# Optimization experiments

Measured on AMD Instinct MI355X. Metric: run time of the kernel, lower is better.

The kernel has to match this reference:

```python
import jax, jax.numpy as jnp
import numpy as np

N_NODES = 100000
N_EDGES = 1600000
IN_DIM = 23
HID_DIM = 128
OUT_DIM = 64
NUM_GRAPHS = 64
EPS = 1e-12


def setup_inputs() -> dict:
    key = jax.random.key(0)
    ks = jax.random.split(key, 8)
    feat_0 = jax.random.normal(ks[0], (N_NODES, IN_DIM), dtype=jnp.float32)
    W1 = jax.random.normal(ks[1], (IN_DIM, HID_DIM), dtype=jnp.float32) * 0.1
    b1 = jax.random.normal(ks[2], (HID_DIM,), dtype=jnp.float32) * 0.1
    W2 = jax.random.normal(ks[3], (HID_DIM, OUT_DIM), dtype=jnp.float32) * 0.1
    b2 = jax.random.normal(ks[4], (OUT_DIM,), dtype=jnp.float32) * 0.1
    src = jax.random.randint(ks[5], (N_EDGES,), 0, N_NODES, dtype=jnp.int64 if jax.config.jax_enable_x64 else jnp.int32)
    dst = jax.random.randint(ks[6], (N_EDGES,), 0, N_NODES, dtype=src.dtype)
    graph_ids = jnp.sort(jax.random.randint(ks[7], (N_NODES,), 0, NUM_GRAPHS, dtype=src.dtype))
    return {"feat_0": feat_0, "W1": W1, "b1": b1, "W2": W2, "b2": b2,
            "src": src, "dst": dst, "graph_ids": graph_ids}


def _sage_gcn(h, src, dst, W, b):
    # DGL SAGEConv with aggregator_type='gcn':
    # h_neigh[v] = (sum_{u->v} h[u] + h[v]) / (in_deg(v) + 1); out = h_neigh @ W + b
    n = h.shape[0]
    agg = jax.ops.segment_sum(h[src], dst, num_segments=n)          # [N, d]
    deg = jax.ops.segment_sum(jnp.ones_like(dst, dtype=h.dtype), dst, num_segments=n)
    h_neigh = (agg + h) / (deg + 1.0)[:, None]
    return h_neigh @ W + b


def reference(feat_0, W1, b1, W2, b2, src, dst, graph_ids):
    # layer 1 + relu + L2 row-normalize (dropout omitted: eval mode)
    h = _sage_gcn(feat_0, src, dst, W1, b1)
    h = jax.nn.relu(h)
    norm = jnp.maximum(jnp.linalg.norm(h, axis=1, keepdims=True), EPS)
    h = h / norm
    # output layer
    h = _sage_gcn(h, src, dst, W2, b2)
    # dgl.mean_nodes: per-graph mean over nodes
    gsum = jax.ops.segment_sum(h, graph_ids, num_segments=NUM_GRAPHS)  # [G, out]
    cnt = jax.ops.segment_sum(jnp.ones((h.shape[0],), h.dtype), graph_ids, num_segments=NUM_GRAPHS)
    return gsum / jnp.maximum(cnt, 1.0)[:, None]
```

## Files before the change

### kernel.cpp

```cpp
#include <hip/hip_runtime.h>

#define IN_DIM 23
#define HID 128
#define OUTD 64
#define NGR 64
#define NXCD 8
#define FB_DIM 32
#define PH_STRIDE 136
#define A2_BLOCKS 2048
#define NB 256
#define CAP 8192
#define CHUNK 4096

typedef __attribute__((ext_vector_type(8))) short bf16x8;
typedef __attribute__((ext_vector_type(4))) float f32x4;
typedef __attribute__((ext_vector_type(2))) float f32x2;

static __device__ __forceinline__ unsigned xcd_id() {
    unsigned x;
    asm volatile("s_getreg_b32 %0, hwreg(20, 0, 32)" : "=s"(x));
    return x & (NXCD - 1);
}

static __device__ __forceinline__ unsigned short f2bf(float x) {
    unsigned u = __float_as_uint(x);
    unsigned r = (u + 0x7FFFu + ((u >> 16) & 1u)) >> 16;
    return (unsigned short)r;
}
static __device__ __forceinline__ float bf2f(unsigned short u) {
    return __uint_as_float((unsigned)u << 16);
}

static __device__ __forceinline__ unsigned enc_fp8(float x) {
    float a = fabsf(x);
    unsigned s = (__float_as_uint(x) >> 31) << 7;
    if (!(a > 0.f)) return s;
    a = fminf(a, 448.f);
    int eb; float fr = frexpf(a, &eb);
    int E = eb - 1;
    int code;
    if (E < -6) code = (int)rintf(ldexpf(a, 9));
    else        code = ((E + 7) << 3) + (int)rintf(ldexpf(fr, 4)) - 8;
    code = min(code, 0x7E);
    return s | (unsigned)code;
}

#if __has_builtin(__builtin_amdgcn_cvt_pk_fp8_f32)
static __device__ __forceinline__ unsigned enc4_fp8(float a, float b,
                                                    float c, float d) {
    int r = __builtin_amdgcn_cvt_pk_fp8_f32(a, b, 0, false);
    r = __builtin_amdgcn_cvt_pk_fp8_f32(c, d, r, true);
    return (unsigned)r;
}
#else
static __device__ __forceinline__ unsigned enc4_fp8(float a, float b,
                                                    float c, float d) {
    return enc_fp8(a) | (enc_fp8(b) << 8) | (enc_fp8(c) << 16)
         | (enc_fp8(d) << 24);
}
#endif

#if __has_builtin(__builtin_amdgcn_cvt_pk_f32_fp8)
static __device__ __forceinline__ void dec_pk(unsigned u, f32x2& lo, f32x2& hi) {
    lo = __builtin_amdgcn_cvt_pk_f32_fp8((int)u, false);
    hi = __builtin_amdgcn_cvt_pk_f32_fp8((int)u, true);
}
#else
static __device__ __forceinline__ float dec1_fp8(unsigned b) {
    unsigned s = (b & 0x80u) << 24;
    unsigned em = b & 0x7Fu;
    float f = __uint_as_float(s | ((em << 20) + 0x3C000000u));
    if ((b & 0x78u) == 0)
        f = 2.f * f - __uint_as_float(s | 0x3C800000u);
    return f;
}
static __device__ __forceinline__ void dec_pk(unsigned u, f32x2& lo, f32x2& hi) {
    lo[0] = dec1_fp8(u & 0xFF);        lo[1] = dec1_fp8((u >> 8) & 0xFF);
    hi[0] = dec1_fp8((u >> 16) & 0xFF); hi[1] = dec1_fp8(u >> 24);
}
#endif

__global__ __launch_bounds__(256) void k_featb(
    const float* __restrict__ feat0, unsigned short* __restrict__ featb,
    int n_nodes)
{
    int i = blockIdx.x * 256 + threadIdx.x;
    if (i >= n_nodes * FB_DIM) return;
    int v = i >> 5, d = i & (FB_DIM - 1);
    float x = (d < IN_DIM) ? feat0[(size_t)v * IN_DIM + d] : 0.f;
    featb[i] = f2bf(x);
}

__global__ __launch_bounds__(256) void k_wprep(
    const float* __restrict__ W1, const float* __restrict__ W2,
    unsigned short* __restrict__ W1t, unsigned short* __restrict__ W2t)
{
    int i = blockIdx.x * 256 + threadIdx.x;
    if (i < HID * 32) {
        int h = i >> 5, d = i & 31;
        W1t[i] = f2bf((d < IN_DIM) ? W1[d * HID + h] : 0.f);
    } else if (i < HID * 32 + OUTD * HID) {
        int j = i - HID * 32;
        int o = j >> 7, k = j & 127;
        W2t[j] = f2bf(W2[k * OUTD + o]);
    }
}

__global__ __launch_bounds__(256) void k_bin(
    const int* __restrict__ src, const int* __restrict__ dst,
    unsigned* __restrict__ brec, int* __restrict__ bcur,
    int n_edges, int n_nodes)
{
    __shared__ int cnt[NB], offs[NB], cur[NB];
    __shared__ unsigned stage[CHUNK];
    int t = threadIdx.x;
    int e0 = blockIdx.x * CHUNK;
    int e1 = min(e0 + CHUNK, n_edges);
    int myb[16];
    unsigned myrec[16];
    cnt[t] = 0;
    __syncthreads();
#pragma unroll
    for (int k = 0; k < 16; ++k) {
        int e = e0 + k * 256 + t;
        myb[k] = -1;
        if (e < e1) {
            int u = src[e], v = dst[e];
            int b = (v * NB) / n_nodes;
            int vlo = (b * n_nodes + NB - 1) / NB;
            myb[k] = b;
            myrec[k] = (unsigned)u | ((unsigned)(v - vlo) << 17);
            atomicAdd(&cnt[b], 1);
        }
    }
    __syncthreads();
    int c = cnt[t];
    offs[t] = c;
    __syncthreads();
    for (int off = 1; off < NB; off <<= 1) {
        int v = (t >= off) ? offs[t - off] : 0;
        __syncthreads();
        offs[t] += v;
        __syncthreads();
    }
    int excl = offs[t] - c;
    __syncthreads();
    offs[t] = excl;
    cur[t] = excl;
    __syncthreads();
#pragma unroll
    for (int k = 0; k < 16; ++k) {
        if (myb[k] >= 0) {
            int slot = atomicAdd(&cur[myb[k]], 1);
            stage[slot] = myrec[k];
        }
    }
    __syncthreads();
    int cc = cnt[t];
    int gb = 0;
    if (cc > 0) gb = atomicAdd(&bcur[t], cc);
    if (gb + cc > CAP) cc = max(0, CAP - gb);
    unsigned* dp = brec + (size_t)t * CAP + gb;
    int sb = offs[t];
    for (int k = 0; k < cc; ++k) dp[k] = stage[sb + k];
}

__global__ __launch_bounds__(NB) void k_bscan(
    const int* __restrict__ bcur, int* __restrict__ bbase,
    int* __restrict__ rowstart, const int* __restrict__ gids,
    float* __restrict__ gcnt, int n_nodes, int n_edges)
{
    __shared__ int s[NB];
    int t = threadIdx.x;
    int c = min(bcur[t], CAP);
    s[t] = c;
    __syncthreads();
    for (int off = 1; off < NB; off <<= 1) {
        int v = (t >= off) ? s[t - off] : 0;
        __syncthreads();
        s[t] += v;
        __syncthreads();
    }
    bbase[t] = s[t] - c;
    if (t == 0) rowstart[n_nodes] = n_edges;
    if (t < NGR) {
        int g = t;
        int lo = 0, hi = n_nodes;
        while (lo < hi) { int m = (lo + hi) >> 1; if (gids[m] < g) lo = m + 1; else hi = m; }
        int lb = lo;
        lo = 0; hi = n_nodes;
        while (lo < hi) { int m = (lo + hi) >> 1; if (gids[m] < g + 1) lo = m + 1; else hi = m; }
        gcnt[g] = (float)(lo - lb);
    }
}

__global__ __launch_bounds__(256) void k_csr(
    const unsigned* __restrict__ brec, const int* __restrict__ bcur,
    const int* __restrict__ bbase, int* __restrict__ rowstart,
    int* __restrict__ eidx, int n_nodes)
{
    __shared__ int hist[512], scr[256];
    int b = blockIdx.x, t = threadIdx.x;
    int vlo = (b * n_nodes + NB - 1) / NB;
    int vhi = ((b + 1) * n_nodes + NB - 1) / NB;
    int nn = vhi - vlo;
    int bcnt = min(bcur[b], CAP);
    int base = bbase[b];
    for (int i = t; i < nn; i += 256) hist[i] = 0;
    __syncthreads();
    const unsigned* rec = brec + (size_t)b * CAP;
    for (int r = t; r < bcnt; r += 256)
        atomicAdd(&hist[rec[r] >> 17], 1);
    __syncthreads();
    int i0 = 2 * t, i1 = i0 + 1;
    int a0 = (i0 < nn) ? hist[i0] : 0;
    int a1 = (i1 < nn) ? hist[i1] : 0;
    int s2 = a0 + a1;
    scr[t] = s2;
    __syncthreads();
    for (int off = 1; off < 256; off <<= 1) {
        int v = (t >= off) ? scr[t - off] : 0;
        __syncthreads();
        scr[t] += v;
        __syncthreads();
    }
    int excl = scr[t] - s2;
    __syncthreads();
    if (i0 < nn) hist[i0] = excl;
    if (i1 < nn) hist[i1] = excl + a0;
    __syncthreads();
    for (int i = t; i < nn; i += 256) rowstart[vlo + i] = base + hist[i];
    __syncthreads();
    for (int r = t; r < bcnt; r += 256) {
        unsigned e = rec[r];
        int pos = atomicAdd(&hist[e >> 17], 1);
        eidx[base + pos] = (int)(e & 0x1FFFFu);
    }
}

__global__ __launch_bounds__(256) void k_agg1(
    const int* __restrict__ rowstart, const int* __restrict__ eidx,
    const unsigned* __restrict__ fbd, unsigned* __restrict__ hnbd, int n_nodes)
{
    int lane = threadIdx.x & 63;
    int quad = lane >> 4, l15 = lane & 15;
    int wglob = (int)((blockIdx.x * 256u + threadIdx.x) >> 6);
    int vA = wglob * 8 + quad * 2;
    if (vA >= n_nodes) return;
    int vB = vA + 1;
    bool hasB = (vB < n_nodes);
    int eA0 = rowstart[vA], eA1 = rowstart[vA + 1];
    int nA = eA1 - eA0;
    int eB0 = eA1, nB = 0;
    if (hasB) nB = rowstart[vB + 1] - eB0;

    int cA = min(16, nA), cB = min(16, nB);
    int idxA = 0, idxB = 0;
    if (l15 < cA) idxA = eidx[eA0 + l15];
    if (l15 < cB) idxB = eidx[eB0 + l15];
    unsigned uuA[16], uuB[16];
#pragma unroll
    for (int j = 0; j < 16; ++j) {
        int sA = __shfl(idxA, quad * 16 + (j < cA ? j : 0));
        uuA[j] = (j < cA) ? fbd[(size_t)sA * 16 + l15] : 0u;
    }
#pragma unroll
    for (int j = 0; j < 16; ++j) {
        int sB = __shfl(idxB, quad * 16 + (j < cB ? j : 0));
        uuB[j] = (j < cB) ? fbd[(size_t)sB * 16 + l15] : 0u;
    }
    float a0 = 0.f, a1 = 0.f;
#pragma unroll
    for (int j = 0; j < 16; ++j) {
        a0 += bf2f((unsigned short)(uuA[j] & 0xFFFF));
        a1 += bf2f((unsigned short)(uuA[j] >> 16));
    }
    for (int base = 16; base < nA; base += 16) {
        int cnt = min(16, nA - base);
        int idx = 0;
        if (l15 < cnt) idx = eidx[eA0 + base + l15];
#pragma unroll
        for (int j = 0; j < 16; ++j) {
            int s = __shfl(idx, quad * 16 + (j < cnt ? j : 0));
            uuA[j] = (j < cnt) ? fbd[(size_t)s * 16 + l15] : 0u;
        }
#pragma unroll
        for (int j = 0; j < 16; ++j) {
            a0 += bf2f((unsigned short)(uuA[j] & 0xFFFF));
            a1 += bf2f((unsigned short)(uuA[j] >> 16));
        }
    }
    {
        unsigned su = fbd[(size_t)vA * 16 + l15];
        float inv = 1.0f / ((float)nA + 1.0f);
        float r0 = (a0 + bf2f((unsigned short)(su & 0xFFFF))) * inv;
        float r1 = (a1 + bf2f((unsigned short)(su >> 16))) * inv;
        hnbd[(size_t)vA * 16 + l15] =
            (unsigned)f2bf(r0) | ((unsigned)f2bf(r1) << 16);
    }
    if (!hasB) return;
    float b0 = 0.f, b1 = 0.f;
#pragma unroll
    for (int j = 0; j < 16; ++j) {
        b0 += bf2f((unsigned short)(uuB[j] & 0xFFFF));
        b1 += bf2f((unsigned short)(uuB[j] >> 16));
    }
    for (int base = 16; base < nB; base += 16) {
        int cnt = min(16, nB - base);
        int idx = 0;
        if (l15 < cnt) idx = eidx[eB0 + base + l15];
#pragma unroll
        for (int j = 0; j < 16; ++j) {
            int s = __shfl(idx, quad * 16 + (j < cnt ? j : 0));
            uuB[j] = (j < cnt) ? fbd[(size_t)s * 16 + l15] : 0u;
        }
#pragma unroll
        for (int j = 0; j < 16; ++j) {
            b0 += bf2f((unsigned short)(uuB[j] & 0xFFFF));
            b1 += bf2f((unsigned short)(uuB[j] >> 16));
        }
    }
    {
        unsigned su = fbd[(size_t)vB * 16 + l15];
        float inv = 1.0f / ((float)nB + 1.0f);
        float r0 = (b0 + bf2f((unsigned short)(su & 0xFFFF))) * inv;
        float r1 = (b1 + bf2f((unsigned short)(su >> 16))) * inv;
        hnbd[(size_t)vB * 16 + l15] =
            (unsigned)f2bf(r0) | ((unsigned)f2bf(r1) << 16);
    }
}

__global__ __launch_bounds__(256) void k_node(
    const unsigned short* __restrict__ hnb, const unsigned short* __restrict__ W1t,
    const float* __restrict__ b1, const unsigned short* __restrict__ W2t,
    unsigned* __restrict__ m1f8, int n_nodes)
{
    __shared__ unsigned short ph[4][16 * PH_STRIDE];
    int wave = threadIdx.x >> 6, lane = threadIdx.x & 63;
    int quad = lane >> 4, l15 = lane & 15;
    const f32x4 z4 = {0.f, 0.f, 0.f, 0.f};

    float bb[8];
#pragma unroll
    for (int t = 0; t < 8; ++t) bb[t] = b1[t * 16 + l15];

    for (int v0 = blockIdx.x * 64 + wave * 16; v0 < n_nodes; v0 += gridDim.x * 64) {
        bf16x8 aH = {0, 0, 0, 0, 0, 0, 0, 0};
        int vA = v0 + l15;
        if (vA < n_nodes) aH = *(const bf16x8*)&hnb[(size_t)vA * FB_DIM + quad * 8];
        f32x4 c1[8];
#pragma unroll
        for (int t = 0; t < 8; ++t) {
            bf16x8 bw = *(const bf16x8*)&W1t[(t * 16 + l15) * 32 + quad * 8];
            c1[t] = __builtin_amdgcn_mfma_f32_16x16x32_bf16(aH, bw, z4, 0, 0, 0);
        }
        float ssq[4] = {0.f, 0.f, 0.f, 0.f};
#pragma unroll
        for (int t = 0; t < 8; ++t) {
#pragma unroll
            for (int r = 0; r < 4; ++r) {
                float x = fmaxf(c1[t][r] + bb[t], 0.f);
                c1[t][r] = x;
                ssq[r] += x * x;
            }
        }
#pragma unroll
        for (int off = 1; off < 16; off <<= 1) {
#pragma unroll
            for (int r = 0; r < 4; ++r) ssq[r] += __shfl_xor(ssq[r], off);
        }
        float inv[4];
#pragma unroll
        for (int r = 0; r < 4; ++r) inv[r] = 1.0f / fmaxf(sqrtf(ssq[r]), 1e-12f);
#pragma unroll
        for (int t = 0; t < 8; ++t)
#pragma unroll
            for (int r = 0; r < 4; ++r)
                ph[wave][(quad * 4 + r) * PH_STRIDE + t * 16 + l15] =
                    f2bf(c1[t][r] * inv[r]);
        f32x4 c2[4] = {z4, z4, z4, z4};
#pragma unroll
        for (int ks = 0; ks < 4; ++ks) {
            bf16x8 aP = *(const bf16x8*)&ph[wave][l15 * PH_STRIDE + ks * 32 + quad * 8];
#pragma unroll
            for (int tn = 0; tn < 4; ++tn) {
                bf16x8 bw = *(const bf16x8*)&W2t[(tn * 16 + l15) * HID + ks * 32 + quad * 8];
                c2[tn] = __builtin_amdgcn_mfma_f32_16x16x32_bf16(aP, bw, c2[tn], 0, 0, 0);
            }
        }
#pragma unroll
        for (int r = 0; r < 4; ++r) {
            int v = v0 + quad * 4 + r;
            if (v < n_nodes) {
                unsigned pk = enc4_fp8(c2[0][r], c2[1][r], c2[2][r], c2[3][r]);
                m1f8[(size_t)v * 16 + l15] = pk;
            }
        }
    }
}

__global__ __launch_bounds__(256) void k_agg2g(
    const int* __restrict__ rowstart, const int* __restrict__ eidx,
    const unsigned* __restrict__ md, const int* __restrict__ gids,
    float* __restrict__ gpart, int n_nodes)
{
    __shared__ float lsum[NGR * OUTD];
    int per = (n_nodes + (int)gridDim.x - 1) / (int)gridDim.x;
    int v_lo = blockIdx.x * per;
    int v_hi = min(v_lo + per, n_nodes);
    if (v_lo >= n_nodes) return;
    int g_lo = gids[v_lo], g_hi = gids[v_hi - 1];
    for (int i = g_lo * OUTD + threadIdx.x; i < (g_hi + 1) * OUTD; i += 256)
        lsum[i] = 0.f;
    __syncthreads();

    int lane = threadIdx.x & 63;
    int wave = threadIdx.x >> 6;
    int quad = lane >> 4, l15 = lane & 15;
    int curg = -1;
    f32x2 c01 = {0.f, 0.f}, c23 = {0.f, 0.f};
    for (int vb = v_lo + wave * 8; vb < v_hi; vb += 32) {
        int vA = vb + quad * 2;
        if (vA >= v_hi) continue;
        int vB = vA + 1;
        bool hasB = (vB < v_hi);
        int eA0 = rowstart[vA], eA1 = rowstart[vA + 1];
        int nA = eA1 - eA0;
        int eB0 = eA1, nB = 0;
        if (hasB) nB = rowstart[vB + 1] - eB0;

        int cA = min(16, nA), cB = min(16, nB);
        int idxA = 0, idxB = 0;
        if (l15 < cA) idxA = eidx[eA0 + l15];
        if (l15 < cB) idxB = eidx[eB0 + l15];
        unsigned uuA[16], uuB[16];
#pragma unroll
        for (int j = 0; j < 16; ++j) {
            int s = __shfl(idxA, quad * 16 + (j < cA ? j : 0));
            uuA[j] = (j < cA) ? md[(size_t)s * 16 + l15] : 0u;
        }
#pragma unroll
        for (int j = 0; j < 16; ++j) {
            int s = __shfl(idxB, quad * 16 + (j < cB ? j : 0));
            uuB[j] = (j < cB) ? md[(size_t)s * 16 + l15] : 0u;
        }
        f32x2 a01 = {0.f, 0.f}, a23 = {0.f, 0.f};
#pragma unroll
        for (int j = 0; j < 16; ++j) {
            f32x2 lo, hi;
            dec_pk(uuA[j], lo, hi);
            a01 += lo; a23 += hi;
        }
        for (int base = 16; base < nA; base += 16) {
            int cnt = min(16, nA - base);
            int idx = 0;
            if (l15 < cnt) idx = eidx[eA0 + base + l15];
#pragma unroll
            for (int j = 0; j < 16; ++j) {
                int s = __shfl(idx, quad * 16 + (j < cnt ? j : 0));
                uuA[j] = (j < cnt) ? md[(size_t)s * 16 + l15] : 0u;
            }
#pragma unroll
            for (int j = 0; j < 16; ++j) {
                f32x2 lo, hi;
                dec_pk(uuA[j], lo, hi);
                a01 += lo; a23 += hi;
            }
        }
        {
            f32x2 lo, hi;
            dec_pk(md[(size_t)vA * 16 + l15], lo, hi);
            a01 += lo; a23 += hi;
        }
        {
            float inv = 1.0f / ((float)nA + 1.0f);
            int g = gids[vA];
            if (g != curg) {
                if (curg >= 0) {
                    atomicAdd(&lsum[curg * OUTD + l15 +  0], c01[0]);
                    atomicAdd(&lsum[curg * OUTD + l15 + 16], c01[1]);
                    atomicAdd(&lsum[curg * OUTD + l15 + 32], c23[0]);
                    atomicAdd(&lsum[curg * OUTD + l15 + 48], c23[1]);
                }
                curg = g;
                c01[0] = a01[0] * inv; c01[1] = a01[1] * inv;
                c23[0] = a23[0] * inv; c23[1] = a23[1] * inv;
            } else {
                c01[0] += a01[0] * inv; c01[1] += a01[1] * inv;
                c23[0] += a23[0] * inv; c23[1] += a23[1] * inv;
            }
        }
        if (!hasB) continue;
        f32x2 b01 = {0.f, 0.f}, b23 = {0.f, 0.f};
#pragma unroll
        for (int j = 0; j < 16; ++j) {
            f32x2 lo, hi;
            dec_pk(uuB[j], lo, hi);
            b01 += lo; b23 += hi;
        }
        for (int base = 16; base < nB; base += 16) {
            int cnt = min(16, nB - base);
            int idx = 0;
            if (l15 < cnt) idx = eidx[eB0 + base + l15];
#pragma unroll
            for (int j = 0; j < 16; ++j) {
                int s = __shfl(idx, quad * 16 + (j < cnt ? j : 0));
                uuB[j] = (j < cnt) ? md[(size_t)s * 16 + l15] : 0u;
            }
#pragma unroll
            for (int j = 0; j < 16; ++j) {
                f32x2 lo, hi;
                dec_pk(uuB[j], lo, hi);
                b01 += lo; b23 += hi;
            }
        }
        {
            f32x2 lo, hi;
            dec_pk(md[(size_t)vB * 16 + l15], lo, hi);
            b01 += lo; b23 += hi;
        }
        {
            float inv = 1.0f / ((float)nB + 1.0f);
            int g = gids[vB];
            if (g != curg) {
                if (curg >= 0) {
                    atomicAdd(&lsum[curg * OUTD + l15 +  0], c01[0]);
                    atomicAdd(&lsum[curg * OUTD + l15 + 16], c01[1]);
                    atomicAdd(&lsum[curg * OUTD + l15 + 32], c23[0]);
                    atomicAdd(&lsum[curg * OUTD + l15 + 48], c23[1]);
                }
                curg = g;
                c01[0] = b01[0] * inv; c01[1] = b01[1] * inv;
                c23[0] = b23[0] * inv; c23[1] = b23[1] * inv;
            } else {
                c01[0] += b01[0] * inv; c01[1] += b01[1] * inv;
                c23[0] += b23[0] * inv; c23[1] += b23[1] * inv;
            }
        }
    }
    if (curg >= 0) {
        atomicAdd(&lsum[curg * OUTD + l15 +  0], c01[0]);
        atomicAdd(&lsum[curg * OUTD + l15 + 16], c01[1]);
        atomicAdd(&lsum[curg * OUTD + l15 + 32], c23[0]);
        atomicAdd(&lsum[curg * OUTD + l15 + 48], c23[1]);
    }
    __syncthreads();
    float* gp = gpart + (size_t)xcd_id() * NGR * OUTD;
    for (int i = g_lo * OUTD + threadIdx.x; i < (g_hi + 1) * OUTD; i += 256)
        atomicAdd(&gp[i], lsum[i]);
}

__global__ __launch_bounds__(256) void k_final(
    const float* __restrict__ gpart, const float* __restrict__ gcnt,
    const float* __restrict__ b2, float* __restrict__ out)
{
    int i = blockIdx.x * 256 + threadIdx.x;
    if (i >= NGR * OUTD) return;
    int g = i >> 6, d = i & 63;
    float s = 0.f;
#pragma unroll
    for (int p = 0; p < NXCD; ++p) s += gpart[(size_t)p * NGR * OUTD + i];
    float c = gcnt[g];
    out[i] = (c > 0.f) ? (s / c + b2[d]) : 0.f;
}

extern "C" void kernel_launch(void* const* d_in, const int* in_sizes, int n_in,
                              void* d_out, int out_size, void* d_ws, size_t ws_size,
                              hipStream_t stream) {
    const float* feat0 = (const float*)d_in[0];
    const float* W1    = (const float*)d_in[1];
    const float* b1    = (const float*)d_in[2];
    const float* W2    = (const float*)d_in[3];
    const float* b2    = (const float*)d_in[4];
    const int*   src   = (const int*)d_in[5];
    const int*   dst   = (const int*)d_in[6];
    const int*   gids  = (const int*)d_in[7];
    int n_edges = in_sizes[5];
    int n_nodes = in_sizes[7];

    unsigned short* W1t = (unsigned short*)d_ws;
    unsigned short* W2t = W1t + HID * 32;
    unsigned short* featb = W2t + (size_t)OUTD * HID;
    unsigned* m1f8 = (unsigned*)featb;
    char* up = (char*)(featb + (size_t)n_nodes * FB_DIM);
    up = (char*)(((uintptr_t)up + 15) & ~(uintptr_t)15);
    unsigned short* hnb = (unsigned short*)up;
    unsigned* brec = (unsigned*)up;
    size_t usz = (size_t)n_nodes * FB_DIM * 2;
    size_t rsz = (size_t)NB * CAP * 4;
    char* after = up + (usz > rsz ? usz : rsz);
    after = (char*)(((uintptr_t)after + 15) & ~(uintptr_t)15);
    int*   eidx     = (int*)after;
    int*   rowstart = eidx + n_edges;
    int*   bcur     = rowstart + n_nodes + 1;
    int*   bbase    = bcur + NB;
    float* gpart    = (float*)(bbase + NB);
    float* gcnt     = gpart + (size_t)NXCD * NGR * OUTD;

    size_t zero_units = 2 * NB + (size_t)NXCD * NGR * OUTD + NGR;
    hipMemsetAsync(bcur, 0, zero_units * 4, stream);

    k_featb<<<(unsigned)(((long long)n_nodes * FB_DIM + 255) / 256), 256, 0, stream>>>(
        feat0, featb, n_nodes);
    k_wprep<<<(HID * 32 + OUTD * HID + 255) / 256, 256, 0, stream>>>(W1, W2, W1t, W2t);

    unsigned blkB = (unsigned)((n_edges + CHUNK - 1) / CHUNK);
    k_bin<<<blkB, 256, 0, stream>>>(src, dst, brec, bcur, n_edges, n_nodes);
    k_bscan<<<1, NB, 0, stream>>>(bcur, bbase, rowstart, gids, gcnt,
                                  n_nodes, n_edges);
    k_csr<<<NB, 256, 0, stream>>>(brec, bcur, bbase, rowstart, eidx, n_nodes);

    unsigned blkA = (unsigned)((n_nodes + 31) / 32);
    k_agg1<<<blkA, 256, 0, stream>>>(rowstart, eidx, (const unsigned*)featb,
                                     (unsigned*)hnb, n_nodes);

    unsigned blkN = (unsigned)((n_nodes + 63) / 64);
    k_node<<<blkN, 256, 0, stream>>>(hnb, W1t, b1, W2t, m1f8, n_nodes);

    k_agg2g<<<A2_BLOCKS, 256, 0, stream>>>(rowstart, eidx, m1f8, gids, gpart,
                                           n_nodes);

    k_final<<<(NGR * OUTD + 255) / 256, 256, 0, stream>>>(gpart, gcnt, b2,
                                                          (float*)d_out);
}
```

Before: 227.3 us.

## Merge prep kernels, coalesce bin scatter, use nontemporal edge-index loads

Fuses the feature and weight bf16 conversion kernels into one launch to save a kernel launch. The bin kernel now writes staged records cooperatively: each thread finds its record's bin by binary search over offsets, so consecutive threads write consecutive addresses instead of each thread serially copying its own bin. Edge-index loads in both aggregation kernels use nontemporal hints to avoid polluting cache that the gathered feature rows need. The binary search adds ALU work per record, and the nontemporal hint may or may not help on this hardware.

Measured after the change: 236.7 us. 4.1% more time.

```diff
diff --git a/kernel.cpp b/kernel.cpp
--- a/kernel.cpp
+++ b/kernel.cpp
@@ -80,29 +80,28 @@
 }
 #endif
 
-__global__ __launch_bounds__(256) void k_featb(
+__global__ __launch_bounds__(256) void k_prep(
     const float* __restrict__ feat0, unsigned short* __restrict__ featb,
+    const float* __restrict__ W1, const float* __restrict__ W2,
+    unsigned short* __restrict__ W1t, unsigned short* __restrict__ W2t,
     int n_nodes)
 {
     int i = blockIdx.x * 256 + threadIdx.x;
-    if (i >= n_nodes * FB_DIM) return;
-    int v = i >> 5, d = i & (FB_DIM - 1);
-    float x = (d < IN_DIM) ? feat0[(size_t)v * IN_DIM + d] : 0.f;
-    featb[i] = f2bf(x);
-}
-
-__global__ __launch_bounds__(256) void k_wprep(
-    const float* __restrict__ W1, const float* __restrict__ W2,
-    unsigned short* __restrict__ W1t, unsigned short* __restrict__ W2t)
-{
-    int i = blockIdx.x * 256 + threadIdx.x;
-    if (i < HID * 32) {
-        int h = i >> 5, d = i & 31;
-        W1t[i] = f2bf((d < IN_DIM) ? W1[d * HID + h] : 0.f);
-    } else if (i < HID * 32 + OUTD * HID) {
-        int j = i - HID * 32;
-        int o = j >> 7, k = j & 127;
-        W2t[j] = f2bf(W2[k * OUTD + o]);
+    int nf = n_nodes * FB_DIM;
+    if (i < nf) {
+        int v = i >> 5, d = i & (FB_DIM - 1);
+        float x = (d < IN_DIM) ? feat0[(size_t)v * IN_DIM + d] : 0.f;
+        featb[i] = f2bf(x);
+    } else {
+        int j = i - nf;
+        if (j < HID * 32) {
+            int h = j >> 5, d = j & 31;
+            W1t[j] = f2bf((d < IN_DIM) ? W1[d * HID + h] : 0.f);
+        } else if (j < HID * 32 + OUTD * HID) {
+            int q = j - HID * 32;
+            int o = q >> 7, k = q & 127;
+            W2t[q] = f2bf(W2[k * OUTD + o]);
+        }
     }
 }
 
@@ -111,11 +110,12 @@
     unsigned* __restrict__ brec, int* __restrict__ bcur,
     int n_edges, int n_nodes)
 {
-    __shared__ int cnt[NB], offs[NB], cur[NB];
+    __shared__ int cnt[NB], offs[NB], cur[NB], gbs[NB];
     __shared__ unsigned stage[CHUNK];
     int t = threadIdx.x;
     int e0 = blockIdx.x * CHUNK;
     int e1 = min(e0 + CHUNK, n_edges);
+    int total = e1 - e0;
     int myb[16];
     unsigned myrec[16];
     cnt[t] = 0;
@@ -155,14 +155,22 @@
             stage[slot] = myrec[k];
         }
     }
-    __syncthreads();
     int cc = cnt[t];
     int gb = 0;
     if (cc > 0) gb = atomicAdd(&bcur[t], cc);
-    if (gb + cc > CAP) cc = max(0, CAP - gb);
-    unsigned* dp = brec + (size_t)t * CAP + gb;
-    int sb = offs[t];
-    for (int k = 0; k < cc; ++k) dp[k] = stage[sb + k];
+    gbs[t] = gb;
+    __syncthreads();
+    for (int r = t; r < total; r += 256) {
+        int lo = 0, hi = NB - 1;
+        while (lo < hi) {
+            int m = (lo + hi + 1) >> 1;
+            if (offs[m] <= r) lo = m; else hi = m - 1;
+        }
+        int k = r - offs[lo];
+        int base = gbs[lo];
+        if (base + k < CAP)
+            brec[(size_t)lo * CAP + base + k] = stage[r];
+    }
 }
 
 __global__ __launch_bounds__(NB) void k_bscan(
@@ -256,8 +264,8 @@
 
     int cA = min(16, nA), cB = min(16, nB);
     int idxA = 0, idxB = 0;
-    if (l15 < cA) idxA = eidx[eA0 + l15];
-    if (l15 < cB) idxB = eidx[eB0 + l15];
+    if (l15 < cA) idxA = __builtin_nontemporal_load(&eidx[eA0 + l15]);
+    if (l15 < cB) idxB = __builtin_nontemporal_load(&eidx[eB0 + l15]);
     unsigned uuA[16], uuB[16];
 #pragma unroll
     for (int j = 0; j < 16; ++j) {
@@ -278,7 +286,7 @@
     for (int base = 16; base < nA; base += 16) {
         int cnt = min(16, nA - base);
         int idx = 0;
-        if (l15 < cnt) idx = eidx[eA0 + base + l15];
+        if (l15 < cnt) idx = __builtin_nontemporal_load(&eidx[eA0 + base + l15]);
 #pragma unroll
         for (int j = 0; j < 16; ++j) {
             int s = __shfl(idx, quad * 16 + (j < cnt ? j : 0));
@@ -308,7 +316,7 @@
     for (int base = 16; base < nB; base += 16) {
         int cnt = min(16, nB - base);
         int idx = 0;
-        if (l15 < cnt) idx = eidx[eB0 + base + l15];
+        if (l15 < cnt) idx = __builtin_nontemporal_load(&eidx[eB0 + base + l15]);
 #pragma unroll
         for (int j = 0; j < 16; ++j) {
             int s = __shfl(idx, quad * 16 + (j < cnt ? j : 0));
@@ -431,8 +439,8 @@
 
         int cA = min(16, nA), cB = min(16, nB);
         int idxA = 0, idxB = 0;
-        if (l15 < cA) idxA = eidx[eA0 + l15];
-        if (l15 < cB) idxB = eidx[eB0 + l15];
+        if (l15 < cA) idxA = __builtin_nontemporal_load(&eidx[eA0 + l15]);
+        if (l15 < cB) idxB = __builtin_nontemporal_load(&eidx[eB0 + l15]);
         unsigned uuA[16], uuB[16];
 #pragma unroll
         for (int j = 0; j < 16; ++j) {
@@ -454,7 +462,7 @@
         for (int base = 16; base < nA; base += 16) {
             int cnt = min(16, nA - base);
             int idx = 0;
-            if (l15 < cnt) idx = eidx[eA0 + base + l15];
+            if (l15 < cnt) idx = __builtin_nontemporal_load(&eidx[eA0 + base + l15]);
 #pragma unroll
             for (int j = 0; j < 16; ++j) {
                 int s = __shfl(idx, quad * 16 + (j < cnt ? j : 0));
@@ -501,7 +509,7 @@
         for (int base = 16; base < nB; base += 16) {
             int cnt = min(16, nB - base);
             int idx = 0;
-            if (l15 < cnt) idx = eidx[eB0 + base + l15];
+            if (l15 < cnt) idx = __builtin_nontemporal_load(&eidx[eB0 + base + l15]);
 #pragma unroll
             for (int j = 0; j < 16; ++j) {
                 int s = __shfl(idx, quad * 16 + (j < cnt ? j : 0));
@@ -600,9 +608,9 @@
     size_t zero_units = 2 * NB + (size_t)NXCD * NGR * OUTD + NGR;
     hipMemsetAsync(bcur, 0, zero_units * 4, stream);
 
-    k_featb<<<(unsigned)(((long long)n_nodes * FB_DIM + 255) / 256), 256, 0, stream>>>(
-        feat0, featb, n_nodes);
-    k_wprep<<<(HID * 32 + OUTD * HID + 255) / 256, 256, 0, stream>>>(W1, W2, W1t, W2t);
+    long long prep_items = (long long)n_nodes * FB_DIM + HID * 32 + OUTD * HID;
+    k_prep<<<(unsigned)((prep_items + 255) / 256), 256, 0, stream>>>(
+        feat0, featb, W1, W2, W1t, W2t, n_nodes);
 
     unsigned blkB = (unsigned)((n_edges + CHUNK - 1) / CHUNK);
     k_bin<<<blkB, 256, 0, stream>>>(src, dst, brec, bcur, n_edges, n_nodes);
```
